# Optimization experiments

Hardware: AMD Instinct MI355X
Metric: run time of the kernel (lower is better)

Reference implementation:

```python
import jax, jax.numpy as jnp
import numpy as np
import math

B, T, O = 4, 1024, 128
D, H, L, V = 512, 8, 6, 128
M, EH = 100000, 4
EHD = D // EH
HD = D // H
TK = O + 2 * T
PAD_ID = 0
NGRAM = 4

def _primes():
    ps = []
    base = 131
    for h in range(EH):
        x = base + h * 1009
        row = []
        for _ in range(NGRAM):
            row.append(x % (2 ** 32))
            x = x * 31 + 1
        ps.append(row)
    return jnp.array(ps, dtype=jnp.uint32)

PRIMES = _primes()

def rmsnorm(x, scale, eps=1e-6):
    return x / jnp.sqrt(jnp.mean(jnp.square(x), axis=-1, keepdims=True) + eps) * scale

def precompute_freqs_cis(dim, max_len, theta=10000.0):
    freqs = 1.0 / theta ** (jnp.arange(0, dim, 2, dtype=jnp.float32) / dim)
    t = jnp.arange(max_len, dtype=jnp.float32)
    return jnp.exp(1j * jnp.outer(t, freqs))[None, :, None, :]  # (1, max_len, 1, dim/2)

def apply_rope(x, f):
    b, t, h, d = x.shape
    xc = jax.lax.complex(x[..., 0::2], x[..., 1::2])
    xr = xc * f
    return jnp.stack([xr.real, xr.imag], axis=-1).reshape(b, t, h, d)

def setup_inputs() -> dict:
    key = jax.random.key(0)
    ks = jax.random.split(key, 16)
    rn = lambda k, shp, s=0.02: jax.random.normal(k, shp, jnp.float32) * s
    logit = lambda p: float(np.log(p / (1.0 - p)))
    return {
        'tokens_w': jax.random.randint(ks[0], (B, T), 0, V, dtype=jnp.int32),
        'mem_ids': jax.random.randint(ks[1], (B, O), 0, V, dtype=jnp.int32),
        'mem_emb': jax.random.normal(ks[2], (B, O, D), jnp.float32),
        'ssum': jax.random.normal(ks[3], (B, D), jnp.float32),
        'embed_table': rn(ks[4], (V, D)),
        'engram_table': rn(ks[5], (M, EH, EHD)),
        'engram_gate': jnp.full((EH, EHD), -2.0, jnp.float32),
        'engram_scale': jnp.ones(D, jnp.float32),
        'mem_W': rn(ks[6], (D, D)), 'mem_b': jnp.zeros(D, jnp.float32),
        'mem_scale': jnp.ones(D, jnp.float32),
        'alpha_gate': jnp.full((D,), logit(0.1), jnp.float32),
        'ssum_W': rn(ks[7], (D, D)),
        'ln1': jnp.ones((L, D), jnp.float32),
        'qW': rn(ks[8], (L, D, D)), 'qb': jnp.zeros((L, D), jnp.float32),
        'kW': rn(ks[9], (L, D, D)), 'kb': jnp.zeros((L, D), jnp.float32),
        'vW': rn(ks[10], (L, D, D)), 'vb': jnp.zeros((L, D), jnp.float32),
        'oW': rn(ks[11], (L, D, D)), 'ob': jnp.zeros((L, D), jnp.float32),
        'ln2': jnp.ones((L, D), jnp.float32),
        'w_in': rn(ks[12], (L, D, 8 * D)),
        'w_out': rn(ks[13], (L, 4 * D, D)),
        'final_scale': jnp.ones(D, jnp.float32),
    }

def _forward(tokens_w, mem_ids, mem_emb, ssum, embed_table, engram_table, engram_gate,
             engram_scale, mem_W, mem_b, mem_scale, alpha_gate, ssum_W,
             ln1, qW, qb, kW, kb, vW, vb, oW, ob, ln2, w_in, w_out, final_scale):
    # token embedding
    x = embed_table[tokens_w]  # (B,T,D)
    # multi-head engram: rolling n-gram hash lookup
    cur = jnp.where(tokens_w == PAD_ID, 0, tokens_w).astype(jnp.uint32)
    prev = jnp.where(mem_ids == PAD_ID, 0, mem_ids).astype(jnp.uint32)
    full = jnp.concatenate([prev, cur], axis=1)  # (B, O+T)
    hs = jnp.zeros((B, T, EH), jnp.uint32)
    for i in range(NGRAM):
        chunk = full[:, O - i: O + T - i]
        hs = hs + chunk[:, :, None] * PRIMES[None, None, :, i]
    idx = (hs % jnp.uint32(M)).astype(jnp.int32)  # (B,T,EH)
    retr = engram_table[idx, jnp.arange(EH)[None, None, :], :]  # (B,T,EH,EHD)
    eng = (retr * jax.nn.sigmoid(engram_gate)[None, None]).reshape(B, T, D)
    eng = rmsnorm(eng, engram_scale)
    # memory adapter + state-sum injection
    mem_p = rmsnorm(mem_emb @ mem_W + mem_b, mem_scale)
    alpha = jax.nn.sigmoid(alpha_gate)
    x = x + (ssum @ ssum_W)[:, None, :] * alpha[None, None, :]
    kv_seq = jnp.concatenate([mem_p, eng, x], axis=1)  # (B, TK, D)
    # masks: mem fully visible, engram + current causal; pad invalid keys
    tril = jnp.tril(jnp.ones((T, T), bool))
    full_mask = jnp.concatenate([jnp.ones((T, O), bool), tril, tril], axis=1)
    valid_curr = tokens_w != PAD_ID
    valid_k = jnp.concatenate([jnp.ones((B, O), bool), valid_curr, valid_curr], axis=1)
    mask = full_mask[None, None] & valid_k[:, None, None, :]  # (B,1,T,TK)
    freqs = precompute_freqs_cis(HD, TK + 32)
    fq, fk = freqs[:, :T], freqs[:, :TK]
    scale = 1.0 / math.sqrt(HD)

    def block(cx, p):
        ln1_, qW_, qb_, kW_, kb_, vW_, vb_, oW_, ob_, ln2_, wi_, wo_ = p
        nx = rmsnorm(cx, ln1_)
        q = (nx @ qW_ + qb_).reshape(B, T, H, HD)
        k = (kv_seq @ kW_ + kb_).reshape(B, TK, H, HD)
        v = (kv_seq @ vW_ + vb_).reshape(B, TK, H, HD)
        q = apply_rope(q, fq)
        k = apply_rope(k, fk)
        scores = jnp.einsum('bqhd,bkhd->bhqk', q, k) * scale
        scores = jnp.where(mask, scores, -1e9)
        probs = jax.nn.softmax(scores, axis=-1)
        o = jnp.einsum('bhqk,bkhd->bqhd', probs, v).reshape(B, T, D)
        cx = cx + o @ oW_ + ob_
        n2 = rmsnorm(cx, ln2_)
        gate, val = jnp.split(n2 @ wi_, 2, axis=-1)
        cx = cx + (jax.nn.silu(gate) * val) @ wo_
        return cx, None

    curr_x, _ = jax.lax.scan(block, x, (ln1, qW, qb, kW, kb, vW, vb, oW, ob, ln2, w_in, w_out))
    return rmsnorm(curr_x, final_scale)

def reference(tokens_w, mem_ids, mem_emb, ssum, embed_table, engram_table, engram_gate,
              engram_scale, mem_W, mem_b, mem_scale, alpha_gate, ssum_W,
              ln1, qW, qb, kW, kb, vW, vb, oW, ob, ln2, w_in, w_out, final_scale):
    return _forward(tokens_w, mem_ids, mem_emb, ssum, embed_table, engram_table, engram_gate,
                    engram_scale, mem_W, mem_b, mem_scale, alpha_gate, ssum_W,
                    ln1, qW, qb, kW, kb, vW, vb, oW, ob, ln2, w_in, w_out, final_scale)
```

## Files before the change

kernel.cpp:

```cpp
#include <hip/hip_runtime.h>
#include <hip/hip_bf16.h>
#include <math.h>

#define B_ 4
#define T_ 1024
#define O_ 128
#define D_ 512
#define H_ 8
#define L_ 6
#define TK_ 2176
#define MM_ 100000
#define EH_ 4
#define EHD_ 128
#define HD_ 64

typedef float f32x4 __attribute__((ext_vector_type(4)));
typedef short bf16x8 __attribute__((ext_vector_type(8)));
typedef unsigned short u16;

__device__ __constant__ unsigned int PRIMES_[4][4] = {
  {131u,  4062u,  125923u, 3903614u},
  {1140u, 35341u, 1095572u, 33962733u},
  {2149u, 66620u, 2065221u, 64021852u},
  {3158u, 97899u, 3034870u, 94080971u},
};

__device__ __forceinline__ float wave_sum_f(float v) {
  #pragma unroll
  for (int off = 32; off; off >>= 1) v += __shfl_xor(v, off);
  return v;
}

__device__ __forceinline__ short f2bf(float f) {
  unsigned int u = __float_as_uint(f);
  unsigned int r = (u + 0x7fffu + ((u >> 16) & 1u)) >> 16;
  return (short)r;
}

__device__ __forceinline__ void gload16(const void* g, void* l) {
  __builtin_amdgcn_global_load_lds((const __attribute__((address_space(1))) void*)g,
                                   (__attribute__((address_space(3))) void*)l, 16, 0, 0);
}

__global__ __launch_bounds__(64) void rope_table_k(float* __restrict__ rc,
                                                   float* __restrict__ rs) {
  int i = blockIdx.x * 64 + threadIdx.x;
  int t = i >> 5, j = i & 31;
  float freq = __powf(10000.0f, -(float)j / 32.0f);
  float ang = (float)t * freq;
  rc[i] = cosf(ang);
  rs[i] = sinf(ang);
}

__global__ __launch_bounds__(256) void ssum_proj_k(const float* __restrict__ ssum,
                                                   const float* __restrict__ sW,
                                                   float* __restrict__ ssp) {
  int col = blockIdx.x * 256 + threadIdx.x;
  int b = blockIdx.y;
  float acc = 0.f;
  for (int d = 0; d < D_; ++d) acc += ssum[b * D_ + d] * sW[(size_t)d * D_ + col];
  ssp[b * D_ + col] = acc;
}

__global__ __launch_bounds__(256) void sgemm_k(const float* __restrict__ A,
                                               const float* __restrict__ W,
                                               const float* __restrict__ bias,
                                               float* __restrict__ C,
                                               int M, int N, int K) {
  __shared__ float As[16][68];
  __shared__ float Bs[16][68];
  int tid = threadIdx.x;
  int row0 = blockIdx.y * 64;
  int col0 = blockIdx.x * 64;
  int tx = tid & 15, ty = tid >> 4;
  int am = tid >> 2, ak = (tid & 3) * 4;
  int bk = tid >> 4, bc = (tid & 15) * 4;
  float acc[4][4] = {};
  for (int k0 = 0; k0 < K; k0 += 16) {
    float4 av = *reinterpret_cast<const float4*>(&A[(size_t)(row0 + am) * K + k0 + ak]);
    As[ak + 0][am] = av.x; As[ak + 1][am] = av.y; As[ak + 2][am] = av.z; As[ak + 3][am] = av.w;
    float4 bv = *reinterpret_cast<const float4*>(&W[(size_t)(k0 + bk) * N + col0 + bc]);
    *reinterpret_cast<float4*>(&Bs[bk][bc]) = bv;
    __syncthreads();
    #pragma unroll
    for (int kk = 0; kk < 16; ++kk) {
      float4 a4 = *reinterpret_cast<const float4*>(&As[kk][ty * 4]);
      float4 b4 = *reinterpret_cast<const float4*>(&Bs[kk][tx * 4]);
      float a[4] = {a4.x, a4.y, a4.z, a4.w};
      float b[4] = {b4.x, b4.y, b4.z, b4.w};
      #pragma unroll
      for (int i = 0; i < 4; ++i)
        #pragma unroll
        for (int j = 0; j < 4; ++j) acc[i][j] += a[i] * b[j];
    }
    __syncthreads();
  }
  int cbase = col0 + tx * 4;
  float4 b4 = *reinterpret_cast<const float4*>(&bias[cbase]);
  float bb[4] = {b4.x, b4.y, b4.z, b4.w};
  #pragma unroll
  for (int i = 0; i < 4; ++i) {
    int row = row0 + ty * 4 + i;
    *reinterpret_cast<float4*>(&C[(size_t)row * N + cbase]) =
        make_float4(acc[i][0] + bb[0], acc[i][1] + bb[1], acc[i][2] + bb[2], acc[i][3] + bb[3]);
  }
}

__device__ __forceinline__ void wconv_tile(const float* __restrict__ W, u16* __restrict__ wT,
                                           int K, int N) {
  __shared__ float s[64][65];
  int n0 = blockIdx.x * 64, k0 = blockIdx.y * 64;
  int tid = threadIdx.x;
  int kr = tid >> 4, nc = (tid & 15) * 4;
  #pragma unroll
  for (int kk = 0; kk < 4; ++kk) {
    float4 f = *reinterpret_cast<const float4*>(&W[(size_t)(k0 + kr + kk * 16) * N + n0 + nc]);
    s[kr + kk * 16][nc + 0] = f.x; s[kr + kk * 16][nc + 1] = f.y;
    s[kr + kk * 16][nc + 2] = f.z; s[kr + kk * 16][nc + 3] = f.w;
  }
  __syncthreads();
  int nr = tid >> 4, kc = (tid & 15) * 4;
  #pragma unroll
  for (int nn = 0; nn < 4; ++nn) {
    int n = nr + nn * 16;
    ushort4 o;
    o.x = (u16)f2bf(s[kc + 0][n]); o.y = (u16)f2bf(s[kc + 1][n]);
    o.z = (u16)f2bf(s[kc + 2][n]); o.w = (u16)f2bf(s[kc + 3][n]);
    *reinterpret_cast<ushort4*>(&wT[(size_t)(n0 + n) * K + k0 + kc]) = o;
  }
}

__global__ __launch_bounds__(256) void wconv_qkvo_k(const float* __restrict__ qW,
                                                    const float* __restrict__ kW,
                                                    const float* __restrict__ vW,
                                                    const float* __restrict__ oW,
                                                    u16* __restrict__ dst) {
  int z = blockIdx.z;
  int l = z >> 2, which = z & 3;
  const float* src = which == 0 ? qW : which == 1 ? kW : which == 2 ? vW : oW;
  wconv_tile(src + (size_t)l * D_ * D_, dst + (size_t)z * D_ * D_, D_, D_);
}

__global__ __launch_bounds__(256) void wconv_win_k(const float* __restrict__ w_in,
                                                   u16* __restrict__ dst) {
  int l = blockIdx.z;
  wconv_tile(w_in + (size_t)l * 512 * 4096, dst + (size_t)l * 4096 * 512, 512, 4096);
}

__global__ __launch_bounds__(256) void wconv_wout_k(const float* __restrict__ w_out,
                                                    u16* __restrict__ dst) {
  int l = blockIdx.z;
  wconv_tile(w_out + (size_t)l * 2048 * 512, dst + (size_t)l * 512 * 2048, 2048, 512);
}

template<int EPI, int MI>
__global__ __launch_bounds__(256) void gemm_bf16_k(const u16* __restrict__ A,
                                                   const u16* __restrict__ Bt,
                                                   const float* __restrict__ bias,
                                                   void* __restrict__ Cout,
                                                   int M, int N, int K, int posmod,
                                                   const float* __restrict__ rc,
                                                   const float* __restrict__ rs) {
  __shared__ __align__(16) u16 As[2][MI * 32 * 32];
  __shared__ __align__(16) u16 Bs[2][128 * 32];
  int tid = threadIdx.x;
  int w = tid >> 6, lane = tid & 63;
  int lr = lane & 15, lg = lane >> 4;
  int row0 = blockIdx.y * (MI * 32), col0 = blockIdx.x * 128;
  int wr = w >> 1, wc = w & 1;
  f32x4 acc[MI][4] = {};

  int srow = lane >> 2;
  int skel = (lane & 3) * 8;

  auto stage = [&](int buf, int k0) {
    if constexpr (MI == 4) {
      #pragma unroll
      for (int ci = 0; ci < 2; ++ci) {
        int c = w * 2 + ci;
        gload16(A + (size_t)(row0 + c * 16 + srow) * K + k0 + skel, &As[buf][c * 512]);
      }
    } else {
      gload16(A + (size_t)(row0 + w * 16 + srow) * K + k0 + skel, &As[buf][w * 512]);
    }
    #pragma unroll
    for (int ci = 0; ci < 2; ++ci) {
      int c = w * 2 + ci;
      gload16(Bt + (size_t)(col0 + c * 16 + srow) * K + k0 + skel, &Bs[buf][c * 512]);
    }
  };

  stage(0, 0);
  __syncthreads();
  int nk = K >> 5;
  int buf = 0;
  for (int t = 0; t < nk; ++t) {
    if (t + 1 < nk) stage(buf ^ 1, (t + 1) * 32);
    bf16x8 af[MI], bfr[4];
    #pragma unroll
    for (int i = 0; i < MI; ++i)
      af[i] = *reinterpret_cast<const bf16x8*>(
          &As[buf][(wr * (16 * MI) + i * 16 + lr) * 32 + lg * 8]);
    #pragma unroll
    for (int j = 0; j < 4; ++j)
      bfr[j] = *reinterpret_cast<const bf16x8*>(&Bs[buf][(wc * 64 + j * 16 + lr) * 32 + lg * 8]);
    #pragma unroll
    for (int i = 0; i < MI; ++i)
      #pragma unroll
      for (int j = 0; j < 4; ++j)
        acc[i][j] = __builtin_amdgcn_mfma_f32_16x16x32_bf16(af[i], bfr[j], acc[i][j], 0, 0, 0);
    __syncthreads();
    buf ^= 1;
  }

  #pragma unroll
  for (int j = 0; j < 4; ++j) {
    int col = col0 + wc * 64 + j * 16 + lr;
    float bs = bias ? bias[col] : 0.f;
    #pragma unroll
    for (int i = 0; i < MI; ++i) {
      #pragma unroll
      for (int r = 0; r < 4; ++r) {
        int row = row0 + wr * (16 * MI) + i * 16 + lg * 4 + r;
        float v = acc[i][j][r] + bs;
        if (EPI == 1) {
          int pos = row % posmod;
          int d = col & 63;
          float c = rc[(size_t)pos * 32 + (d >> 1)];
          float s = rs[(size_t)pos * 32 + (d >> 1)];
          float partner = __shfl_xor(v, 1);
          v = (d & 1) ? (partner * s + v * c) : (v * c - partner * s);
        }
        if (EPI == 2) {
          float* Cf = (float*)Cout;
          Cf[(size_t)row * N + col] += v;
        } else {
          u16* Cb = (u16*)Cout;
          Cb[(size_t)row * N + col] = (u16)f2bf(v);
        }
      }
    }
  }
}

__global__ __launch_bounds__(256) void kv_gemm_k(const u16* __restrict__ A,
                                                 const u16* __restrict__ wkT,
                                                 const u16* __restrict__ wvT,
                                                 const float* __restrict__ kbias,
                                                 const float* __restrict__ vbias,
                                                 u16* __restrict__ kb,
                                                 u16* __restrict__ vb,
                                                 const float* __restrict__ rc,
                                                 const float* __restrict__ rs) {
  __shared__ __align__(16) u16 As[2][128 * 32];
  __shared__ __align__(16) u16 Bk[2][64 * 32];
  __shared__ __align__(16) u16 Bv[2][64 * 32];
  const int K = 512, N = 512;
  int tid = threadIdx.x;
  int w = tid >> 6, lane = tid & 63;
  int lr = lane & 15, lg = lane >> 4;
  int row0 = blockIdx.y * 128, col0 = blockIdx.x * 64;
  int wr = w >> 1, wc = w & 1;
  f32x4 ak_[4][2] = {};
  f32x4 av_[4][2] = {};

  int srow = lane >> 2;
  int skel = (lane & 3) * 8;

  auto stage = [&](int buf, int k0) {
    #pragma unroll
    for (int ci = 0; ci < 2; ++ci) {
      int c = w * 2 + ci;
      gload16(A + (size_t)(row0 + c * 16 + srow) * K + k0 + skel, &As[buf][c * 512]);
    }
    gload16(wkT + (size_t)(col0 + w * 16 + srow) * K + k0 + skel, &Bk[buf][w * 512]);
    gload16(wvT + (size_t)(col0 + w * 16 + srow) * K + k0 + skel, &Bv[buf][w * 512]);
  };

  stage(0, 0);
  __syncthreads();
  int buf = 0;
  for (int t = 0; t < 16; ++t) {
    if (t + 1 < 16) stage(buf ^ 1, (t + 1) * 32);
    bf16x8 af[4], bk[2], bv[2];
    #pragma unroll
    for (int i = 0; i < 4; ++i)
      af[i] = *reinterpret_cast<const bf16x8*>(&As[buf][(wr * 64 + i * 16 + lr) * 32 + lg * 8]);
    #pragma unroll
    for (int j = 0; j < 2; ++j) {
      bk[j] = *reinterpret_cast<const bf16x8*>(&Bk[buf][(wc * 32 + j * 16 + lr) * 32 + lg * 8]);
      bv[j] = *reinterpret_cast<const bf16x8*>(&Bv[buf][(wc * 32 + j * 16 + lr) * 32 + lg * 8]);
    }
    #pragma unroll
    for (int i = 0; i < 4; ++i)
      #pragma unroll
      for (int j = 0; j < 2; ++j) {
        ak_[i][j] = __builtin_amdgcn_mfma_f32_16x16x32_bf16(af[i], bk[j], ak_[i][j], 0, 0, 0);
        av_[i][j] = __builtin_amdgcn_mfma_f32_16x16x32_bf16(af[i], bv[j], av_[i][j], 0, 0, 0);
      }
    __syncthreads();
    buf ^= 1;
  }

  #pragma unroll
  for (int j = 0; j < 2; ++j) {
    int col = col0 + wc * 32 + j * 16 + lr;
    float kbs = kbias[col], vbs = vbias[col];
    int d = col & 63;
    #pragma unroll
    for (int i = 0; i < 4; ++i) {
      #pragma unroll
      for (int r = 0; r < 4; ++r) {
        int row = row0 + wr * 64 + i * 16 + lg * 4 + r;
        int pos = row % TK_;
        float vk = ak_[i][j][r] + kbs;
        float c = rc[(size_t)pos * 32 + (d >> 1)];
        float s = rs[(size_t)pos * 32 + (d >> 1)];
        float partner = __shfl_xor(vk, 1);
        vk = (d & 1) ? (partner * s + vk * c) : (vk * c - partner * s);
        kb[(size_t)row * N + col] = (u16)f2bf(vk);
        vb[(size_t)row * N + col] = (u16)f2bf(av_[i][j][r] + vbs);
      }
    }
  }
}

__global__ __launch_bounds__(256) void mlp_in_mfma_k(const u16* __restrict__ A,
                                                     const u16* __restrict__ wiT,
                                                     u16* __restrict__ Hout) {
  __shared__ __align__(16) u16 As[2][128 * 32];
  __shared__ __align__(16) u16 Bg[2][64 * 32];
  __shared__ __align__(16) u16 Bv[2][64 * 32];
  int tid = threadIdx.x;
  int w = tid >> 6, lane = tid & 63;
  int lr = lane & 15, lg = lane >> 4;
  int hc0 = blockIdx.x * 64, row0 = blockIdx.y * 128;
  int wr = w >> 1, wc = w & 1;
  f32x4 ag[4][2] = {};
  f32x4 av[4][2] = {};
  const int K = 512;

  int srow = lane >> 2;
  int skel = (lane & 3) * 8;

  auto stage = [&](int buf, int k0) {
    #pragma unroll
    for (int ci = 0; ci < 2; ++ci) {
      int c = w * 2 + ci;
      gload16(A + (size_t)(row0 + c * 16 + srow) * K + k0 + skel, &As[buf][c * 512]);
    }
    gload16(wiT + (size_t)(hc0 + w * 16 + srow) * K + k0 + skel, &Bg[buf][w * 512]);
    gload16(wiT + (size_t)(2048 + hc0 + w * 16 + srow) * K + k0 + skel, &Bv[buf][w * 512]);
  };

  stage(0, 0);
  __syncthreads();
  int buf = 0;
  for (int t = 0; t < 16; ++t) {
    if (t + 1 < 16) stage(buf ^ 1, (t + 1) * 32);
    bf16x8 af[4], bg[2], bv[2];
    #pragma unroll
    for (int i = 0; i < 4; ++i)
      af[i] = *reinterpret_cast<const bf16x8*>(&As[buf][(wr * 64 + i * 16 + lr) * 32 + lg * 8]);
    #pragma unroll
    for (int j = 0; j < 2; ++j) {
      bg[j] = *reinterpret_cast<const bf16x8*>(&Bg[buf][(wc * 32 + j * 16 + lr) * 32 + lg * 8]);
      bv[j] = *reinterpret_cast<const bf16x8*>(&Bv[buf][(wc * 32 + j * 16 + lr) * 32 + lg * 8]);
    }
    #pragma unroll
    for (int i = 0; i < 4; ++i)
      #pragma unroll
      for (int j = 0; j < 2; ++j) {
        ag[i][j] = __builtin_amdgcn_mfma_f32_16x16x32_bf16(af[i], bg[j], ag[i][j], 0, 0, 0);
        av[i][j] = __builtin_amdgcn_mfma_f32_16x16x32_bf16(af[i], bv[j], av[i][j], 0, 0, 0);
      }
    __syncthreads();
    buf ^= 1;
  }

  #pragma unroll
  for (int j = 0; j < 2; ++j) {
    int col = hc0 + wc * 32 + j * 16 + lr;
    #pragma unroll
    for (int i = 0; i < 4; ++i) {
      #pragma unroll
      for (int r = 0; r < 4; ++r) {
        int row = row0 + wr * 64 + i * 16 + lg * 4 + r;
        float g = ag[i][j][r];
        float sg = g / (1.f + __expf(-g));
        Hout[(size_t)row * 2048 + col] = (u16)f2bf(sg * av[i][j][r]);
      }
    }
  }
}

template<int OUTBF>
__global__ __launch_bounds__(128) void rmsnorm_k(const float* __restrict__ in,
                                                 const float* __restrict__ scale,
                                                 void* __restrict__ out) {
  int row = blockIdx.x;
  int tid = threadIdx.x;
  float4 v = *reinterpret_cast<const float4*>(&in[(size_t)row * D_ + tid * 4]);
  float ss = v.x * v.x + v.y * v.y + v.z * v.z + v.w * v.w;
  ss = wave_sum_f(ss);
  __shared__ float red[2];
  if ((tid & 63) == 0) red[tid >> 6] = ss;
  __syncthreads();
  ss = red[0] + red[1];
  float inv = 1.0f / sqrtf(ss / (float)D_ + 1e-6f);
  float4 sc = *reinterpret_cast<const float4*>(&scale[tid * 4]);
  float o0 = v.x * inv * sc.x, o1 = v.y * inv * sc.y, o2 = v.z * inv * sc.z, o3 = v.w * inv * sc.w;
  if (OUTBF) {
    ushort4 o;
    o.x = (u16)f2bf(o0); o.y = (u16)f2bf(o1); o.z = (u16)f2bf(o2); o.w = (u16)f2bf(o3);
    *reinterpret_cast<ushort4*>((u16*)out + (size_t)row * D_ + tid * 4) = o;
  } else {
    *reinterpret_cast<float4*>((float*)out + (size_t)row * D_ + tid * 4) =
        make_float4(o0, o1, o2, o3);
  }
}

__global__ __launch_bounds__(128) void memnorm_k(const float* __restrict__ tmp,
                                                 const float* __restrict__ scale,
                                                 u16* __restrict__ kv) {
  int o = blockIdx.x, b = blockIdx.y;
  int tid = threadIdx.x;
  float4 v = *reinterpret_cast<const float4*>(&tmp[(size_t)(b * O_ + o) * D_ + tid * 4]);
  float ss = v.x * v.x + v.y * v.y + v.z * v.z + v.w * v.w;
  ss = wave_sum_f(ss);
  __shared__ float red[2];
  if ((tid & 63) == 0) red[tid >> 6] = ss;
  __syncthreads();
  ss = red[0] + red[1];
  float inv = 1.0f / sqrtf(ss / (float)D_ + 1e-6f);
  float4 sc = *reinterpret_cast<const float4*>(&scale[tid * 4]);
  ushort4 oo;
  oo.x = (u16)f2bf(v.x * inv * sc.x); oo.y = (u16)f2bf(v.y * inv * sc.y);
  oo.z = (u16)f2bf(v.z * inv * sc.z); oo.w = (u16)f2bf(v.w * inv * sc.w);
  *reinterpret_cast<ushort4*>(&kv[(size_t)(b * TK_ + o) * D_ + tid * 4]) = oo;
}

__global__ __launch_bounds__(128) void engram_k(const int* __restrict__ tokens,
                                                const int* __restrict__ mem_ids,
                                                const float* __restrict__ etab,
                                                const float* __restrict__ egate,
                                                const float* __restrict__ escale,
                                                u16* __restrict__ kv) {
  int t = blockIdx.x, b = blockIdx.y;
  int tid = threadIdx.x;
  unsigned int toks[4];
  #pragma unroll
  for (int i = 0; i < 4; ++i) {
    int idx = t - i;
    toks[i] = (idx >= 0) ? (unsigned int)tokens[b * T_ + idx]
                         : (unsigned int)mem_ids[b * O_ + O_ + idx];
  }
  int c = tid * 4;
  int h = c >> 7;
  int e = c & 127;
  unsigned int hs = 0;
  #pragma unroll
  for (int i = 0; i < 4; ++i) hs += toks[i] * PRIMES_[h][i];
  int idxh = (int)(hs % (unsigned int)MM_);
  float4 r = *reinterpret_cast<const float4*>(&etab[((size_t)idxh * EH_ + h) * EHD_ + e]);
  float4 g = *reinterpret_cast<const float4*>(&egate[h * EHD_ + e]);
  float4 val;
  val.x = r.x / (1.f + __expf(-g.x));
  val.y = r.y / (1.f + __expf(-g.y));
  val.z = r.z / (1.f + __expf(-g.z));
  val.w = r.w / (1.f + __expf(-g.w));
  float ss = val.x * val.x + val.y * val.y + val.z * val.z + val.w * val.w;
  ss = wave_sum_f(ss);
  __shared__ float red[2];
  if ((tid & 63) == 0) red[tid >> 6] = ss;
  __syncthreads();
  ss = red[0] + red[1];
  float inv = 1.0f / sqrtf(ss / (float)D_ + 1e-6f);
  float4 sc = *reinterpret_cast<const float4*>(&escale[c]);
  ushort4 oo;
  oo.x = (u16)f2bf(val.x * inv * sc.x); oo.y = (u16)f2bf(val.y * inv * sc.y);
  oo.z = (u16)f2bf(val.z * inv * sc.z); oo.w = (u16)f2bf(val.w * inv * sc.w);
  *reinterpret_cast<ushort4*>(&kv[(size_t)(b * TK_ + O_ + t) * D_ + c]) = oo;
}

__global__ __launch_bounds__(128) void embed_k(const int* __restrict__ tokens,
                                               const float* __restrict__ etab,
                                               const float* __restrict__ ssp,
                                               const float* __restrict__ alpha_g,
                                               float* __restrict__ cx,
                                               u16* __restrict__ kv) {
  int t = blockIdx.x, b = blockIdx.y;
  int tid = threadIdx.x;
  int c = tid * 4;
  int tok = tokens[b * T_ + t];
  float4 e = *reinterpret_cast<const float4*>(&etab[(size_t)tok * D_ + c]);
  float4 sp = *reinterpret_cast<const float4*>(&ssp[b * D_ + c]);
  float4 ag = *reinterpret_cast<const float4*>(&alpha_g[c]);
  float4 x;
  x.x = e.x + sp.x / (1.f + __expf(-ag.x));
  x.y = e.y + sp.y / (1.f + __expf(-ag.y));
  x.z = e.z + sp.z / (1.f + __expf(-ag.z));
  x.w = e.w + sp.w / (1.f + __expf(-ag.w));
  *reinterpret_cast<float4*>(&cx[(size_t)(b * T_ + t) * D_ + c]) = x;
  ushort4 oo;
  oo.x = (u16)f2bf(x.x); oo.y = (u16)f2bf(x.y);
  oo.z = (u16)f2bf(x.z); oo.w = (u16)f2bf(x.w);
  *reinterpret_cast<ushort4*>(&kv[(size_t)(b * TK_ + O_ + T_ + t) * D_ + c]) = oo;
}

#define KIDX8(r, c) (((r) << 6) + ((c) ^ (((r) & 7) << 3)))
#define KIDX4(r, c) (((r) << 6) + ((c) ^ (((r) & 15) << 2)))
#define PIDX(q, o) (((q) << 5) + ((o) ^ (((q) & 7) << 2)))

__global__ __launch_bounds__(256) void attn_mfma_k(const u16* __restrict__ qb,
                                                   const u16* __restrict__ kb,
                                                   const u16* __restrict__ vb,
                                                   const int* __restrict__ tokens,
                                                   u16* __restrict__ ob) {
  __shared__ __align__(16) short ks[2][64 * 64];
  __shared__ __align__(16) short vst[2][64 * 64];
  __shared__ __align__(16) unsigned int pbuf[4][16 * 32];
  __shared__ unsigned char vtok[T_];

  int fid = blockIdx.x;
  int h = fid & 7;
  int s = fid >> 3;
  int b, bx;
  if (s < 32) { bx = s >> 1; b = s & 1; }
  else { int s2 = s - 32; bx = 15 - (s2 >> 1); b = 2 + (s2 & 1); }

  int qt0 = bx * 64;
  int tid = threadIdx.x;
  int w = tid >> 6, lane = tid & 63;
  int lr = lane & 15;
  int lg = lane >> 4;
  int qw0 = qt0 + w * 16;
  int tq = qw0 + lr;

  for (int i = tid; i < T_; i += 256) vtok[i] = (tokens[b * T_ + i] != 0);

  bf16x8 aq[2];
  {
    const u16* qp = &qb[((size_t)(b * T_) + tq) * D_ + h * 64];
    aq[0] = *reinterpret_cast<const bf16x8*>(qp + lg * 8);
    aq[1] = *reinterpret_cast<const bf16x8*>(qp + 32 + lg * 8);
  }

  float m_ = -1e30f, lsum = 0.f;
  f32x4 od[4];
  #pragma unroll
  for (int dt = 0; dt < 4; ++dt) od[dt] = (f32x4){0.f, 0.f, 0.f, 0.f};

  int sr = tid >> 2;
  int sc = (tid & 3) * 16;
  int vr = (tid >> 4) * 4;
  int vc = (tid & 15) * 4;

  int nt = 2 + 2 * (bx + 1);
  auto tile_pos = [&](int i, int& pos0, int& base, bool& masked) {
    if (i < 2) { pos0 = i * 64; base = 0; masked = false; }
    else if (i < 2 + (bx + 1)) { pos0 = O_ + (i - 2) * 64; base = O_; masked = true; }
    else { pos0 = O_ + T_ + (i - 2 - (bx + 1)) * 64; base = O_ + T_; masked = true; }
  };

  bf16x8 pk0, pk1;
  short4 pv0, pv1, pv2, pv3;

  auto load_regs = [&](int pos0) {
    const u16* kg = &kb[((size_t)(b * TK_) + pos0 + sr) * D_ + h * 64 + sc];
    pk0 = *reinterpret_cast<const bf16x8*>(kg);
    pk1 = *reinterpret_cast<const bf16x8*>(kg + 8);
    const u16* vg = &vb[((size_t)(b * TK_) + pos0 + vr) * D_ + h * 64 + vc];
    pv0 = *reinterpret_cast<const short4*>(vg);
    pv1 = *reinterpret_cast<const short4*>(vg + D_);
    pv2 = *reinterpret_cast<const short4*>(vg + 2 * D_);
    pv3 = *reinterpret_cast<const short4*>(vg + 3 * D_);
  };

  auto write_lds = [&](int buf) {
    *reinterpret_cast<bf16x8*>(&ks[buf][KIDX8(sr, sc)]) = pk0;
    *reinterpret_cast<bf16x8*>(&ks[buf][KIDX8(sr, sc + 8)]) = pk1;
    short4 t0 = make_short4(pv0.x, pv1.x, pv2.x, pv3.x);
    short4 t1 = make_short4(pv0.y, pv1.y, pv2.y, pv3.y);
    short4 t2 = make_short4(pv0.z, pv1.z, pv2.z, pv3.z);
    short4 t3 = make_short4(pv0.w, pv1.w, pv2.w, pv3.w);
    *reinterpret_cast<short4*>(&vst[buf][KIDX4(vc + 0, vr)]) = t0;
    *reinterpret_cast<short4*>(&vst[buf][KIDX4(vc + 1, vr)]) = t1;
    *reinterpret_cast<short4*>(&vst[buf][KIDX4(vc + 2, vr)]) = t2;
    *reinterpret_cast<short4*>(&vst[buf][KIDX4(vc + 3, vr)]) = t3;
  };

  unsigned int* pw = (unsigned int*)pbuf[w];

  auto compute = [&](int buf, int pos0, int base, bool masked) {
    float sv[4][4];
    __builtin_amdgcn_s_setprio(1);
    #pragma unroll
    for (int kt = 0; kt < 4; ++kt) {
      bf16x8 ka0 = *reinterpret_cast<const bf16x8*>(&ks[buf][KIDX8(kt * 16 + lr, lg * 8)]);
      bf16x8 ka1 = *reinterpret_cast<const bf16x8*>(&ks[buf][KIDX8(kt * 16 + lr, 32 + lg * 8)]);
      f32x4 sf = (f32x4){0.f, 0.f, 0.f, 0.f};
      sf = __builtin_amdgcn_mfma_f32_16x16x32_bf16(ka0, aq[0], sf, 0, 0, 0);
      sf = __builtin_amdgcn_mfma_f32_16x16x32_bf16(ka1, aq[1], sf, 0, 0, 0);
      #pragma unroll
      for (int r = 0; r < 4; ++r) sv[kt][r] = sf[r];
    }
    __builtin_amdgcn_s_setprio(0);
    if (masked) {
      #pragma unroll
      for (int kt = 0; kt < 4; ++kt) {
        #pragma unroll
        for (int r = 0; r < 4; ++r) {
          int tk = pos0 + kt * 16 + lg * 4 + r - base;
          bool valid = (vtok[tk] != 0) && (tk <= tq);
          sv[kt][r] = valid ? sv[kt][r] * 0.125f : -1e30f;
        }
      }
    } else {
      #pragma unroll
      for (int kt = 0; kt < 4; ++kt)
        #pragma unroll
        for (int r = 0; r < 4; ++r) sv[kt][r] *= 0.125f;
    }
    float pmax = sv[0][0];
    #pragma unroll
    for (int kt = 0; kt < 4; ++kt)
      #pragma unroll
      for (int r = 0; r < 4; ++r) pmax = fmaxf(pmax, sv[kt][r]);
    pmax = fmaxf(pmax, __shfl_xor(pmax, 16));
    pmax = fmaxf(pmax, __shfl_xor(pmax, 32));
    float mnew = fmaxf(m_, pmax);
    float al = __expf(m_ - mnew);
    m_ = mnew;
    float psum = 0.f;
    #pragma unroll
    for (int kt = 0; kt < 4; ++kt)
      #pragma unroll
      for (int r = 0; r < 4; ++r) {
        float pe = __expf(sv[kt][r] - mnew);
        sv[kt][r] = pe;
        psum += pe;
      }
    psum += __shfl_xor(psum, 16);
    psum += __shfl_xor(psum, 32);
    lsum = lsum * al + psum;
    #pragma unroll
    for (int dt = 0; dt < 4; ++dt) {
      f32x4 o = od[dt];
      o[0] *= al; o[1] *= al; o[2] *= al; o[3] *= al;
      od[dt] = o;
    }
    #pragma unroll
    for (int kt = 0; kt < 4; ++kt) {
      uint2 wp;
      asm("v_cvt_pk_bf16_f32 %0, %1, %2" : "=v"(wp.x) : "v"(sv[kt][0]), "v"(sv[kt][1]));
      asm("v_cvt_pk_bf16_f32 %0, %1, %2" : "=v"(wp.y) : "v"(sv[kt][2]), "v"(sv[kt][3]));
      *reinterpret_cast<uint2*>(&pw[PIDX(lr, kt * 8 + lg * 2)]) = wp;
    }
    bf16x8 pf0 = *reinterpret_cast<const bf16x8*>(&pw[PIDX(lr, lg * 4)]);
    bf16x8 pf1 = *reinterpret_cast<const bf16x8*>(&pw[PIDX(lr, 16 + lg * 4)]);
    __builtin_amdgcn_s_setprio(1);
    #pragma unroll
    for (int dt = 0; dt < 4; ++dt) {
      short4 lo0 = *reinterpret_cast<const short4*>(&vst[buf][KIDX4(dt * 16 + lr, lg * 8)]);
      short4 hi0 = *reinterpret_cast<const short4*>(&vst[buf][KIDX4(dt * 16 + lr, lg * 8 + 4)]);
      short4 lo1 = *reinterpret_cast<const short4*>(&vst[buf][KIDX4(dt * 16 + lr, 32 + lg * 8)]);
      short4 hi1 = *reinterpret_cast<const short4*>(&vst[buf][KIDX4(dt * 16 + lr, 36 + lg * 8)]);
      bf16x8 va0 = {lo0.x, lo0.y, lo0.z, lo0.w, hi0.x, hi0.y, hi0.z, hi0.w};
      bf16x8 va1 = {lo1.x, lo1.y, lo1.z, lo1.w, hi1.x, hi1.y, hi1.z, hi1.w};
      od[dt] = __builtin_amdgcn_mfma_f32_16x16x32_bf16(va0, pf0, od[dt], 0, 0, 0);
      od[dt] = __builtin_amdgcn_mfma_f32_16x16x32_bf16(va1, pf1, od[dt], 0, 0, 0);
    }
    __builtin_amdgcn_s_setprio(0);
  };

  {
    int pos0, base; bool masked;
    tile_pos(0, pos0, base, masked);
    load_regs(pos0);
  }
  for (int i = 0; i < nt; ++i) {
    write_lds(i & 1);
    __syncthreads();
    int pos0, base; bool masked;
    tile_pos(i, pos0, base, masked);
    if (i + 1 < nt) {
      int npos, nbase; bool nmask;
      tile_pos(i + 1, npos, nbase, nmask);
      load_regs(npos);
    }
    compute(i & 1, pos0, base, masked);
  }

  float inv = 1.0f / lsum;
  #pragma unroll
  for (int dt = 0; dt < 4; ++dt) {
    ushort4 o4;
    o4.x = (u16)f2bf(od[dt][0] * inv);
    o4.y = (u16)f2bf(od[dt][1] * inv);
    o4.z = (u16)f2bf(od[dt][2] * inv);
    o4.w = (u16)f2bf(od[dt][3] * inv);
    *reinterpret_cast<ushort4*>(
        &ob[((size_t)(b * T_) + tq) * D_ + h * 64 + dt * 16 + lg * 4]) = o4;
  }
}

extern "C" void kernel_launch(void* const* d_in, const int* in_sizes, int n_in,
                              void* d_out, int out_size, void* d_ws, size_t ws_size,
                              hipStream_t stream) {
  (void)in_sizes; (void)n_in; (void)out_size; (void)ws_size;
  const int* tokens = (const int*)d_in[0];
  const int* mem_ids = (const int*)d_in[1];
  const float* mem_emb = (const float*)d_in[2];
  const float* ssum = (const float*)d_in[3];
  const float* embed = (const float*)d_in[4];
  const float* engram_t = (const float*)d_in[5];
  const float* engram_g = (const float*)d_in[6];
  const float* engram_s = (const float*)d_in[7];
  const float* mem_W = (const float*)d_in[8];
  const float* mem_b = (const float*)d_in[9];
  const float* mem_s = (const float*)d_in[10];
  const float* alpha_g = (const float*)d_in[11];
  const float* ssum_W = (const float*)d_in[12];
  const float* ln1 = (const float*)d_in[13];
  const float* qW = (const float*)d_in[14];
  const float* qbias = (const float*)d_in[15];
  const float* kW = (const float*)d_in[16];
  const float* kbias = (const float*)d_in[17];
  const float* vW = (const float*)d_in[18];
  const float* vbias = (const float*)d_in[19];
  const float* oW = (const float*)d_in[20];
  const float* obias = (const float*)d_in[21];
  const float* ln2 = (const float*)d_in[22];
  const float* w_in = (const float*)d_in[23];
  const float* w_out = (const float*)d_in[24];
  const float* final_s = (const float*)d_in[25];

  char* p = (char*)d_ws;
  auto alloc = [&](size_t bytes) { char* r = p; p += (bytes + 255) & ~(size_t)255; return r; };
  u16* kv_b   = (u16*)alloc((size_t)B_ * TK_ * D_ * 2);
  float* cx   = (float*)alloc((size_t)B_ * T_ * D_ * 4);
  u16* nx_b   = (u16*)alloc((size_t)B_ * T_ * D_ * 2);
  u16* qb_b   = (u16*)alloc((size_t)B_ * T_ * D_ * 2);
  u16* kb_b   = (u16*)alloc((size_t)B_ * TK_ * D_ * 2);
  u16* vb_b   = (u16*)alloc((size_t)B_ * TK_ * D_ * 2);
  u16* wqkvoT = (u16*)alloc((size_t)L_ * 4 * D_ * D_ * 2);
  u16* wiT    = (u16*)alloc((size_t)L_ * 4096 * 512 * 2);
  u16* woutT  = (u16*)alloc((size_t)L_ * 512 * 2048 * 2);
  float* ssp  = (float*)alloc((size_t)B_ * D_ * 4);
  float* rc   = (float*)alloc((size_t)TK_ * 32 * 4);
  float* rs   = (float*)alloc((size_t)TK_ * 32 * 4);
  float* mem_tmp = (float*)qb_b;
  u16* ob_b = nx_b;
  u16* hb = kb_b;
  (void)vb_b;

  rope_table_k<<<TK_ * 32 / 64, 64, 0, stream>>>(rc, rs);
  wconv_qkvo_k<<<dim3(8, 8, L_ * 4), 256, 0, stream>>>(qW, kW, vW, oW, wqkvoT);
  wconv_win_k<<<dim3(64, 8, L_), 256, 0, stream>>>(w_in, wiT);
  wconv_wout_k<<<dim3(8, 32, L_), 256, 0, stream>>>(w_out, woutT);
  ssum_proj_k<<<dim3(2, B_), 256, 0, stream>>>(ssum, ssum_W, ssp);
  sgemm_k<<<dim3(8, 8), 256, 0, stream>>>(mem_emb, mem_W, mem_b, mem_tmp, B_ * O_, D_, D_);
  memnorm_k<<<dim3(O_, B_), 128, 0, stream>>>(mem_tmp, mem_s, kv_b);
  engram_k<<<dim3(T_, B_), 128, 0, stream>>>(tokens, mem_ids, engram_t, engram_g, engram_s, kv_b);
  embed_k<<<dim3(T_, B_), 128, 0, stream>>>(tokens, embed, ssp, alpha_g, cx, kv_b);

  const size_t WSZ = (size_t)D_ * D_;
  for (int l = 0; l < L_; ++l) {
    const u16* wqT = wqkvoT + ((size_t)l * 4 + 0) * WSZ;
    const u16* wkT = wqkvoT + ((size_t)l * 4 + 1) * WSZ;
    const u16* wvT = wqkvoT + ((size_t)l * 4 + 2) * WSZ;
    const u16* woT = wqkvoT + ((size_t)l * 4 + 3) * WSZ;
    const u16* wil = wiT + (size_t)l * 4096 * 512;
    const u16* wol = woutT + (size_t)l * 512 * 2048;

    rmsnorm_k<1><<<B_ * T_, 128, 0, stream>>>(cx, ln1 + l * D_, nx_b);
    gemm_bf16_k<1, 2><<<dim3(4, 64), 256, 0, stream>>>(nx_b, wqT, qbias + l * D_, qb_b,
                                                       B_ * T_, D_, D_, T_, rc, rs);
    kv_gemm_k<<<dim3(8, 68), 256, 0, stream>>>(kv_b, wkT, wvT, kbias + l * D_, vbias + l * D_,
                                               kb_b, vb_b, rc, rs);
    attn_mfma_k<<<dim3(512), 256, 0, stream>>>(qb_b, kb_b, vb_b, tokens, ob_b);
    gemm_bf16_k<2, 2><<<dim3(4, 64), 256, 0, stream>>>(ob_b, woT, obias + l * D_, cx,
                                                       B_ * T_, D_, D_, 0, nullptr, nullptr);
    rmsnorm_k<1><<<B_ * T_, 128, 0, stream>>>(cx, ln2 + l * D_, nx_b);
    mlp_in_mfma_k<<<dim3(32, 32), 256, 0, stream>>>(nx_b, wil, hb);
    gemm_bf16_k<2, 2><<<dim3(4, 64), 256, 0, stream>>>(hb, wol, nullptr, cx,
                                                       B_ * T_, D_, 2048, 0, nullptr, nullptr);
  }
  rmsnorm_k<0><<<B_ * T_, 128, 0, stream>>>(cx, final_s, d_out);
}
```

Baseline: 1.285 ms.

## Batch K/V projections across layers and pair causal query tiles per attention block

K/V projections depend only on the fixed kv_b sequence, not on the per-layer residual, so when the workspace is large enough they are computed for all six layers in one launch with a layer grid dimension. The attention kernel now uses 512-thread blocks that pair query tile bx with tile 15-bx, sharing K/V tile loads and skipping compute for tiles beyond each half's causal extent. This balances load and reduces launch count, at the cost of a much larger workspace and some idle waves on the shorter half.

Measured after the change: 1.156 ms. 1.11x faster.

```diff
diff --git a/kernel.cpp b/kernel.cpp
--- a/kernel.cpp
+++ b/kernel.cpp
@@ -244,18 +244,25 @@
 }
 
 __global__ __launch_bounds__(256) void kv_gemm_k(const u16* __restrict__ A,
-                                                 const u16* __restrict__ wkT,
-                                                 const u16* __restrict__ wvT,
-                                                 const float* __restrict__ kbias,
-                                                 const float* __restrict__ vbias,
-                                                 u16* __restrict__ kb,
-                                                 u16* __restrict__ vb,
+                                                 const u16* __restrict__ wqkvoT,
+                                                 const float* __restrict__ kbias_all,
+                                                 const float* __restrict__ vbias_all,
+                                                 u16* __restrict__ kb_base,
+                                                 u16* __restrict__ vb_base,
                                                  const float* __restrict__ rc,
-                                                 const float* __restrict__ rs) {
+                                                 const float* __restrict__ rs,
+                                                 int l0, size_t ostride) {
   __shared__ __align__(16) u16 As[2][128 * 32];
   __shared__ __align__(16) u16 Bk[2][64 * 32];
   __shared__ __align__(16) u16 Bv[2][64 * 32];
   const int K = 512, N = 512;
+  int l = l0 + blockIdx.z;
+  const u16* wkT = wqkvoT + ((size_t)l * 4 + 1) * (D_ * D_);
+  const u16* wvT = wqkvoT + ((size_t)l * 4 + 2) * (D_ * D_);
+  const float* kbias = kbias_all + l * D_;
+  const float* vbias = vbias_all + l * D_;
+  u16* kb = kb_base + (size_t)blockIdx.z * ostride;
+  u16* vb = vb_base + (size_t)blockIdx.z * ostride;
   int tid = threadIdx.x;
   int w = tid >> 6, lane = tid & 63;
   int lr = lane & 15, lg = lane >> 4;
@@ -512,32 +519,32 @@
 #define KIDX4(r, c) (((r) << 6) + ((c) ^ (((r) & 15) << 2)))
 #define PIDX(q, o) (((q) << 5) + ((o) ^ (((q) & 7) << 2)))
 
-__global__ __launch_bounds__(256) void attn_mfma_k(const u16* __restrict__ qb,
+__global__ __launch_bounds__(512) void attn_mfma_k(const u16* __restrict__ qb,
                                                    const u16* __restrict__ kb,
                                                    const u16* __restrict__ vb,
                                                    const int* __restrict__ tokens,
                                                    u16* __restrict__ ob) {
   __shared__ __align__(16) short ks[2][64 * 64];
   __shared__ __align__(16) short vst[2][64 * 64];
-  __shared__ __align__(16) unsigned int pbuf[4][16 * 32];
+  __shared__ __align__(16) unsigned int pbuf[8][16 * 32];
   __shared__ unsigned char vtok[T_];
 
   int fid = blockIdx.x;
   int h = fid & 7;
   int s = fid >> 3;
-  int b, bx;
-  if (s < 32) { bx = s >> 1; b = s & 1; }
-  else { int s2 = s - 32; bx = 15 - (s2 >> 1); b = 2 + (s2 & 1); }
-
-  int qt0 = bx * 64;
+  int pair = s & 7;
+  int b = s >> 3;
+  int bxA = pair, bxB = 15 - pair;
+
   int tid = threadIdx.x;
   int w = tid >> 6, lane = tid & 63;
   int lr = lane & 15;
   int lg = lane >> 4;
-  int qw0 = qt0 + w * 16;
+  int myBx = (w < 4) ? bxA : bxB;
+  int qw0 = myBx * 64 + (w & 3) * 16;
   int tq = qw0 + lr;
 
-  for (int i = tid; i < T_; i += 256) vtok[i] = (tokens[b * T_ + i] != 0);
+  for (int i = tid; i < T_; i += 512) vtok[i] = (tokens[b * T_ + i] != 0);
 
   bf16x8 aq[2];
   {
@@ -551,43 +558,44 @@
   #pragma unroll
   for (int dt = 0; dt < 4; ++dt) od[dt] = (f32x4){0.f, 0.f, 0.f, 0.f};
 
-  int sr = tid >> 2;
-  int sc = (tid & 3) * 16;
-  int vr = (tid >> 4) * 4;
+  int sr = tid >> 3;
+  int sc = (tid & 7) * 8;
+  int vr2 = (tid >> 4) * 2;
   int vc = (tid & 15) * 4;
 
-  int nt = 2 + 2 * (bx + 1);
-  auto tile_pos = [&](int i, int& pos0, int& base, bool& masked) {
-    if (i < 2) { pos0 = i * 64; base = 0; masked = false; }
-    else if (i < 2 + (bx + 1)) { pos0 = O_ + (i - 2) * 64; base = O_; masked = true; }
-    else { pos0 = O_ + T_ + (i - 2 - (bx + 1)) * 64; base = O_ + T_; masked = true; }
+  int nt = 2 + 2 * (bxB + 1);
+  auto tile_pos = [&](int i, int& pos0, int& base, bool& masked, bool& part) {
+    if (i < 2) { pos0 = i * 64; base = 0; masked = false; part = true; }
+    else if (i < 3 + bxB) {
+      int t = i - 2;
+      pos0 = O_ + t * 64; base = O_; masked = true; part = (t <= myBx);
+    } else {
+      int t = i - (3 + bxB);
+      pos0 = O_ + T_ + t * 64; base = O_ + T_; masked = true; part = (t <= myBx);
+    }
   };
 
-  bf16x8 pk0, pk1;
-  short4 pv0, pv1, pv2, pv3;
+  bf16x8 pk0;
+  short4 pv0, pv1;
 
   auto load_regs = [&](int pos0) {
     const u16* kg = &kb[((size_t)(b * TK_) + pos0 + sr) * D_ + h * 64 + sc];
     pk0 = *reinterpret_cast<const bf16x8*>(kg);
-    pk1 = *reinterpret_cast<const bf16x8*>(kg + 8);
-    const u16* vg = &vb[((size_t)(b * TK_) + pos0 + vr) * D_ + h * 64 + vc];
+    const u16* vg = &vb[((size_t)(b * TK_) + pos0 + vr2) * D_ + h * 64 + vc];
     pv0 = *reinterpret_cast<const short4*>(vg);
     pv1 = *reinterpret_cast<const short4*>(vg + D_);
-    pv2 = *reinterpret_cast<const short4*>(vg + 2 * D_);
-    pv3 = *reinterpret_cast<const short4*>(vg + 3 * D_);
   };
 
   auto write_lds = [&](int buf) {
     *reinterpret_cast<bf16x8*>(&ks[buf][KIDX8(sr, sc)]) = pk0;
-    *reinterpret_cast<bf16x8*>(&ks[buf][KIDX8(sr, sc + 8)]) = pk1;
-    short4 t0 = make_short4(pv0.x, pv1.x, pv2.x, pv3.x);
-    short4 t1 = make_short4(pv0.y, pv1.y, pv2.y, pv3.y);
-    short4 t2 = make_short4(pv0.z, pv1.z, pv2.z, pv3.z);
-    short4 t3 = make_short4(pv0.w, pv1.w, pv2.w, pv3.w);
-    *reinterpret_cast<short4*>(&vst[buf][KIDX4(vc + 0, vr)]) = t0;
-    *reinterpret_cast<short4*>(&vst[buf][KIDX4(vc + 1, vr)]) = t1;
-    *reinterpret_cast<short4*>(&vst[buf][KIDX4(vc + 2, vr)]) = t2;
-    *reinterpret_cast<short4*>(&vst[buf][KIDX4(vc + 3, vr)]) = t3;
+    unsigned int t0 = (unsigned int)(u16)pv0.x | ((unsigned int)(u16)pv1.x << 16);
+    unsigned int t1 = (unsigned int)(u16)pv0.y | ((unsigned int)(u16)pv1.y << 16);
+    unsigned int t2 = (unsigned int)(u16)pv0.z | ((unsigned int)(u16)pv1.z << 16);
+    unsigned int t3 = (unsigned int)(u16)pv0.w | ((unsigned int)(u16)pv1.w << 16);
+    *reinterpret_cast<unsigned int*>(&vst[buf][KIDX4(vc + 0, vr2)]) = t0;
+    *reinterpret_cast<unsigned int*>(&vst[buf][KIDX4(vc + 1, vr2)]) = t1;
+    *reinterpret_cast<unsigned int*>(&vst[buf][KIDX4(vc + 2, vr2)]) = t2;
+    *reinterpret_cast<unsigned int*>(&vst[buf][KIDX4(vc + 3, vr2)]) = t3;
   };
 
   unsigned int* pw = (unsigned int*)pbuf[w];
@@ -675,21 +683,21 @@
   };
 
   {
-    int pos0, base; bool masked;
-    tile_pos(0, pos0, base, masked);
+    int pos0, base; bool masked, part;
+    tile_pos(0, pos0, base, masked, part);
     load_regs(pos0);
   }
   for (int i = 0; i < nt; ++i) {
     write_lds(i & 1);
     __syncthreads();
-    int pos0, base; bool masked;
-    tile_pos(i, pos0, base, masked);
+    int pos0, base; bool masked, part;
+    tile_pos(i, pos0, base, masked, part);
     if (i + 1 < nt) {
-      int npos, nbase; bool nmask;
-      tile_pos(i + 1, npos, nbase, nmask);
+      int npos, nbase; bool nmask, npart;
+      tile_pos(i + 1, npos, nbase, nmask, npart);
       load_regs(npos);
     }
-    compute(i & 1, pos0, base, masked);
+    if (part) compute(i & 1, pos0, base, masked);
   }
 
   float inv = 1.0f / lsum;
@@ -708,7 +716,7 @@
 extern "C" void kernel_launch(void* const* d_in, const int* in_sizes, int n_in,
                               void* d_out, int out_size, void* d_ws, size_t ws_size,
                               hipStream_t stream) {
-  (void)in_sizes; (void)n_in; (void)out_size; (void)ws_size;
+  (void)in_sizes; (void)n_in; (void)out_size;
   const int* tokens = (const int*)d_in[0];
   const int* mem_ids = (const int*)d_in[1];
   const float* mem_emb = (const float*)d_in[2];
@@ -736,14 +744,22 @@
   const float* w_out = (const float*)d_in[24];
   const float* final_s = (const float*)d_in[25];
 
+  const size_t KVSZ = (size_t)B_ * TK_ * D_;
+  size_t need = (KVSZ * 2 * 2 * L_) + 120u * 1024 * 1024;
+  bool batched = ws_size >= need;
+
   char* p = (char*)d_ws;
   auto alloc = [&](size_t bytes) { char* r = p; p += (bytes + 255) & ~(size_t)255; return r; };
-  u16* kv_b   = (u16*)alloc((size_t)B_ * TK_ * D_ * 2);
+  u16* kv_b   = (u16*)alloc(KVSZ * 2);
   float* cx   = (float*)alloc((size_t)B_ * T_ * D_ * 4);
   u16* nx_b   = (u16*)alloc((size_t)B_ * T_ * D_ * 2);
   u16* qb_b   = (u16*)alloc((size_t)B_ * T_ * D_ * 2);
-  u16* kb_b   = (u16*)alloc((size_t)B_ * TK_ * D_ * 2);
-  u16* vb_b   = (u16*)alloc((size_t)B_ * TK_ * D_ * 2);
+  int nkv = batched ? L_ : 1;
+  u16* kb_all = (u16*)alloc(KVSZ * 2 * nkv);
+  u16* vb_all = (u16*)alloc(KVSZ * 2 * nkv);
+  u16* hb;
+  if (batched) hb = (u16*)alloc((size_t)B_ * T_ * 2048 * 2);
+  else hb = kb_all;
   u16* wqkvoT = (u16*)alloc((size_t)L_ * 4 * D_ * D_ * 2);
   u16* wiT    = (u16*)alloc((size_t)L_ * 4096 * 512 * 2);
   u16* woutT  = (u16*)alloc((size_t)L_ * 512 * 2048 * 2);
@@ -752,8 +768,6 @@
   float* rs   = (float*)alloc((size_t)TK_ * 32 * 4);
   float* mem_tmp = (float*)qb_b;
   u16* ob_b = nx_b;
-  u16* hb = kb_b;
-  (void)vb_b;
 
   rope_table_k<<<TK_ * 32 / 64, 64, 0, stream>>>(rc, rs);
   wconv_qkvo_k<<<dim3(8, 8, L_ * 4), 256, 0, stream>>>(qW, kW, vW, oW, wqkvoT);
@@ -765,21 +779,28 @@
   engram_k<<<dim3(T_, B_), 128, 0, stream>>>(tokens, mem_ids, engram_t, engram_g, engram_s, kv_b);
   embed_k<<<dim3(T_, B_), 128, 0, stream>>>(tokens, embed, ssp, alpha_g, cx, kv_b);
 
+  if (batched) {
+    kv_gemm_k<<<dim3(8, 68, L_), 256, 0, stream>>>(kv_b, wqkvoT, kbias, vbias,
+                                                   kb_all, vb_all, rc, rs, 0, KVSZ);
+  }
+
   const size_t WSZ = (size_t)D_ * D_;
   for (int l = 0; l < L_; ++l) {
     const u16* wqT = wqkvoT + ((size_t)l * 4 + 0) * WSZ;
-    const u16* wkT = wqkvoT + ((size_t)l * 4 + 1) * WSZ;
-    const u16* wvT = wqkvoT + ((size_t)l * 4 + 2) * WSZ;
     const u16* woT = wqkvoT + ((size_t)l * 4 + 3) * WSZ;
     const u16* wil = wiT + (size_t)l * 4096 * 512;
     const u16* wol = woutT + (size_t)l * 512 * 2048;
+    u16* kb_l = batched ? kb_all + (size_t)l * KVSZ : kb_all;
+    u16* vb_l = batched ? vb_all + (size_t)l * KVSZ : vb_all;
 
     rmsnorm_k<1><<<B_ * T_, 128, 0, stream>>>(cx, ln1 + l * D_, nx_b);
     gemm_bf16_k<1, 2><<<dim3(4, 64), 256, 0, stream>>>(nx_b, wqT, qbias + l * D_, qb_b,
                                                        B_ * T_, D_, D_, T_, rc, rs);
-    kv_gemm_k<<<dim3(8, 68), 256, 0, stream>>>(kv_b, wkT, wvT, kbias + l * D_, vbias + l * D_,
-                                               kb_b, vb_b, rc, rs);
-    attn_mfma_k<<<dim3(512), 256, 0, stream>>>(qb_b, kb_b, vb_b, tokens, ob_b);
+    if (!batched) {
+      kv_gemm_k<<<dim3(8, 68, 1), 256, 0, stream>>>(kv_b, wqkvoT, kbias, vbias,
+                                                    kb_l, vb_l, rc, rs, l, 0);
+    }
+    attn_mfma_k<<<dim3(256), 512, 0, stream>>>(qb_b, kb_l, vb_l, tokens, ob_b);
     gemm_bf16_k<2, 2><<<dim3(4, 64), 256, 0, stream>>>(ob_b, woT, obias + l * D_, cx,
                                                        B_ * T_, D_, D_, 0, nullptr, nullptr);
     rmsnorm_k<1><<<B_ * T_, 128, 0, stream>>>(cx, ln2 + l * D_, nx_b);
```
